# Optimization experiments

Measured on AMD Instinct MI355X. Metric: run time of the kernel, lower is better.

## Reference

```python
import jax, jax.numpy as jnp
import numpy as np

NBLOCK = 2000
DIM = 2048
B, T = 32, 1024
EPS = 1e-12  # F.normalize eps


def _l2norm(v, axis):
    n = jnp.sqrt(jnp.sum(v * v, axis=axis, keepdims=True))
    return v / jnp.maximum(n, EPS)


def setup_inputs() -> dict:
    key = jax.random.key(0)
    kx, km, kw = jax.random.split(key, 3)
    x = jax.random.normal(kx, (B, T, DIM), dtype=jnp.float32)
    mask = jax.random.randint(km, (B, T), 0, 2).astype(jnp.int32)
    stdv = 1.0 / np.sqrt(DIM)
    weight = jax.random.uniform(kw, (NBLOCK, DIM), dtype=jnp.float32,
                                minval=-stdv, maxval=stdv)
    return {"x": x, "mask": mask, "weight": weight}


def reference(x, mask, weight):
    half = x.shape[0] // 2
    nblock = weight.shape[0]
    m = mask.astype(x.dtype)  # [B, T]

    # diversity: || W W^T - I ||_F
    gram = weight @ weight.T  # [N, N]
    diversity_loss = jnp.linalg.norm(gram - jnp.eye(nblock, dtype=weight.dtype))

    # cosine-similarity attention: [B, T, N]
    att = jnp.einsum('btd,nd->btn', _l2norm(x, axis=2), _l2norm(weight, axis=1))

    # uniformity loss: masked sum over T, softmax over blocks, mean over half-batch
    s = jnp.einsum('btn,bt->nb', att[:half], m[:half])  # [N, half]
    tmp = jnp.mean(jax.nn.softmax(s, axis=0), axis=1)   # [N]
    u_loss = jnp.linalg.norm(tmp)

    # per-row min over masked positions of the top-1 similarity
    top1 = jnp.max(att, axis=2)  # [B, T] (only topk[...,0] is used)
    inf = jnp.asarray(jnp.inf, dtype=x.dtype)
    masked_top1 = jnp.where(m > 0, top1, inf)
    min_sim = jnp.min(masked_top1[:half], axis=1)   # [half]
    ab_min = jnp.min(masked_top1[half:], axis=1)    # [half]

    return (0.2 * diversity_loss,
            2.0 - jnp.mean(min_sim) + jnp.mean(ab_min),
            0.5 * u_loss)
```

## Files before the change

kernel.cpp:

```cpp
#include <hip/hip_runtime.h>

typedef unsigned short u16;
typedef unsigned int u32;
typedef __attribute__((ext_vector_type(8))) short short8;
typedef __attribute__((ext_vector_type(8))) u16 ushort8;
typedef __attribute__((ext_vector_type(4))) float fx4;

#define DIMK 2048
#define NBLK 2000

typedef const __attribute__((address_space(1))) void* gp_t;
typedef __attribute__((address_space(3))) void* lp_t;

__device__ __forceinline__ u16 f2bf(float f) {
  u32 u = __float_as_uint(f);
  u32 r = (u + 0x7fffu + ((u >> 16) & 1u)) >> 16;
  return (u16)r;
}

__device__ __forceinline__ u32 fkey(float f) {
  u32 u = __float_as_uint(f);
  return (u & 0x80000000u) ? ~u : (u | 0x80000000u);
}
__device__ __forceinline__ float dekey(u32 k) {
  u32 u = (k & 0x80000000u) ? (k ^ 0x80000000u) : ~k;
  return __uint_as_float(u);
}

__device__ __forceinline__ void gemm_tile(const u16* __restrict__ Abase,
                                          const u16* __restrict__ Bbase,
                                          int row0, int col0,
                                          u16* lsA, u16* lsB,
                                          fx4 acc[4][4])
{
  const int tid  = threadIdx.x;
  const int wv   = tid >> 6;
  const int lane = tid & 63;
  const int wr   = wv & 1, wc = wv >> 1;
  const int quad = lane >> 4, lc = lane & 15;

  const int srow = wv * 32 + (lane >> 2);
  const int skel = (lane & 3) * 8;
  const u16* gA0 = Abase + (size_t)(row0 + srow) * DIMK + skel;
  const u16* gA1 = Abase + (size_t)(row0 + srow + 16) * DIMK + skel;
  const u16* gB0 = Bbase + (size_t)(col0 + srow) * DIMK + skel;
  const u16* gB1 = Bbase + (size_t)(col0 + srow + 16) * DIMK + skel;
  u16* lA0 = lsA + wv * 1024;
  u16* lA1 = lsA + wv * 1024 + 512;
  u16* lB0 = lsB + wv * 1024;
  u16* lB1 = lsB + wv * 1024 + 512;

  const int fA = (wr * 64 + lc) * 32 + quad * 8;
  const int fB = (wc * 64 + lc) * 32 + quad * 8;

#pragma unroll
  for (int mi = 0; mi < 4; mi++)
#pragma unroll
    for (int ni = 0; ni < 4; ni++)
      acc[mi][ni] = fx4{0.f, 0.f, 0.f, 0.f};

  for (int k0 = 0; k0 < DIMK; k0 += 32) {
    __syncthreads();
    __builtin_amdgcn_global_load_lds((gp_t)gA0, (lp_t)lA0, 16, 0, 0);
    __builtin_amdgcn_global_load_lds((gp_t)gA1, (lp_t)lA1, 16, 0, 0);
    __builtin_amdgcn_global_load_lds((gp_t)gB0, (lp_t)lB0, 16, 0, 0);
    __builtin_amdgcn_global_load_lds((gp_t)gB1, (lp_t)lB1, 16, 0, 0);
    gA0 += 32; gA1 += 32; gB0 += 32; gB1 += 32;
    __syncthreads();
    short8 af[4], bfr[4];
#pragma unroll
    for (int mi = 0; mi < 4; mi++)
      af[mi] = *(const short8*)(lsA + fA + mi * 512);
#pragma unroll
    for (int ni = 0; ni < 4; ni++)
      bfr[ni] = *(const short8*)(lsB + fB + ni * 512);
#pragma unroll
    for (int mi = 0; mi < 4; mi++)
#pragma unroll
      for (int ni = 0; ni < 4; ni++)
        acc[mi][ni] = __builtin_amdgcn_mfma_f32_16x16x32_bf16(af[mi], bfr[ni], acc[mi][ni], 0, 0, 0);
  }
}

__global__ __launch_bounds__(256) void norm_rows_x(const float* __restrict__ x,
                                                   u16* __restrict__ Xn)
{
  const int row = blockIdx.x;
  const int tid = threadIdx.x;
  __shared__ float red[4];
  const float4* xr = (const float4*)(x + (size_t)row * DIMK);
  float4 v0 = xr[2 * tid];
  float4 v1 = xr[2 * tid + 1];
  float ss = v0.x*v0.x + v0.y*v0.y + v0.z*v0.z + v0.w*v0.w
           + v1.x*v1.x + v1.y*v1.y + v1.z*v1.z + v1.w*v1.w;
#pragma unroll
  for (int off = 1; off < 64; off <<= 1) ss += __shfl_xor(ss, off);
  if ((tid & 63) == 0) red[tid >> 6] = ss;
  __syncthreads();
  ss = red[0] + red[1] + red[2] + red[3];
  float inv = 1.0f / fmaxf(sqrtf(ss), 1e-12f);
  ushort8 o;
  o[0] = f2bf(v0.x * inv); o[1] = f2bf(v0.y * inv);
  o[2] = f2bf(v0.z * inv); o[3] = f2bf(v0.w * inv);
  o[4] = f2bf(v1.x * inv); o[5] = f2bf(v1.y * inv);
  o[6] = f2bf(v1.z * inv); o[7] = f2bf(v1.w * inv);
  ((ushort8*)(Xn + (size_t)row * DIMK))[tid] = o;
}

__global__ __launch_bounds__(256) void norm_rows_w(const float* __restrict__ w,
                                                   u16* __restrict__ Wn,
                                                   u16* __restrict__ Wb)
{
  const int row = blockIdx.x;
  const int tid = threadIdx.x;
  __shared__ float red[4];
  if (row < NBLK) {
    const float4* wr_ = (const float4*)(w + (size_t)row * DIMK);
    float4 v0 = wr_[2 * tid];
    float4 v1 = wr_[2 * tid + 1];
    float ss = v0.x*v0.x + v0.y*v0.y + v0.z*v0.z + v0.w*v0.w
             + v1.x*v1.x + v1.y*v1.y + v1.z*v1.z + v1.w*v1.w;
#pragma unroll
    for (int off = 1; off < 64; off <<= 1) ss += __shfl_xor(ss, off);
    if ((tid & 63) == 0) red[tid >> 6] = ss;
    __syncthreads();
    ss = red[0] + red[1] + red[2] + red[3];
    float inv = 1.0f / fmaxf(sqrtf(ss), 1e-12f);
    ushort8 on, ob;
    on[0] = f2bf(v0.x * inv); on[1] = f2bf(v0.y * inv);
    on[2] = f2bf(v0.z * inv); on[3] = f2bf(v0.w * inv);
    on[4] = f2bf(v1.x * inv); on[5] = f2bf(v1.y * inv);
    on[6] = f2bf(v1.z * inv); on[7] = f2bf(v1.w * inv);
    ob[0] = f2bf(v0.x); ob[1] = f2bf(v0.y); ob[2] = f2bf(v0.z); ob[3] = f2bf(v0.w);
    ob[4] = f2bf(v1.x); ob[5] = f2bf(v1.y); ob[6] = f2bf(v1.z); ob[7] = f2bf(v1.w);
    ((ushort8*)(Wn + (size_t)row * DIMK))[tid] = on;
    ((ushort8*)(Wb + (size_t)row * DIMK))[tid] = ob;
  } else {
    ushort8 z = ushort8{0, 0, 0, 0, 0, 0, 0, 0};
    ((ushort8*)(Wn + (size_t)row * DIMK))[tid] = z;
    ((ushort8*)(Wb + (size_t)row * DIMK))[tid] = z;
  }
}

__global__ __launch_bounds__(256) void gram_kernel(const u16* __restrict__ Wb,
                                                   float* __restrict__ divsum)
{
  __shared__ __align__(16) u16 lsA[4096];
  __shared__ __align__(16) u16 lsB[4096];
  fx4 acc[4][4];
  const int i0 = blockIdx.y * 128, j0 = blockIdx.x * 128;
  gemm_tile(Wb, Wb, i0, j0, lsA, lsB, acc);
  const int tid = threadIdx.x, wv = tid >> 6, lane = tid & 63;
  const int wr = wv & 1, wc = wv >> 1, quad = lane >> 4, lc = lane & 15;
  float local = 0.f;
#pragma unroll
  for (int mi = 0; mi < 4; mi++) {
#pragma unroll
    for (int ni = 0; ni < 4; ni++) {
#pragma unroll
      for (int r = 0; r < 4; r++) {
        int i = i0 + wr * 64 + mi * 16 + quad * 4 + r;
        int j = j0 + wc * 64 + ni * 16 + lc;
        float g = acc[mi][ni][r];
        float d = (i == j && i < NBLK) ? 1.0f : 0.0f;
        float e = g - d;
        local += e * e;
      }
    }
  }
#pragma unroll
  for (int off = 1; off < 64; off <<= 1) local += __shfl_xor(local, off);
  if (lane == 0) atomicAdd(divsum, local);
}

__global__ __launch_bounds__(256) void att_kernel(const u16* __restrict__ Xn,
                                                  const u16* __restrict__ Wn,
                                                  const int* __restrict__ mask,
                                                  u32* __restrict__ top1k,
                                                  float* __restrict__ s)
{
  __shared__ __align__(16) u16 lsA[4096];
  __shared__ __align__(16) u16 lsB[4096];
  __shared__ float sMask[128];
  const int xb = blockIdx.x, yb = blockIdx.y;
  const int tid = threadIdx.x;
  if (tid < 128) sMask[tid] = (float)mask[yb * 128 + tid];
  fx4 acc[4][4];
  gemm_tile(Xn, Wn, yb * 128, xb * 128, lsA, lsB, acc);
  const int wv = tid >> 6, lane = tid & 63;
  const int wr = wv & 1, wc = wv >> 1, quad = lane >> 4, lc = lane & 15;
  const int colbase = xb * 128 + wc * 64;

#pragma unroll
  for (int mi = 0; mi < 4; mi++) {
#pragma unroll
    for (int r = 0; r < 4; r++) {
      float v = -3.0e38f;
#pragma unroll
      for (int ni = 0; ni < 4; ni++) {
        int col = colbase + ni * 16 + lc;
        float av = acc[mi][ni][r];
        v = (col < NBLK && av > v) ? av : v;
      }
      v = fmaxf(v, __shfl_xor(v, 1));
      v = fmaxf(v, __shfl_xor(v, 2));
      v = fmaxf(v, __shfl_xor(v, 4));
      v = fmaxf(v, __shfl_xor(v, 8));
      if (lc == 0) {
        int row = yb * 128 + wr * 64 + mi * 16 + quad * 4 + r;
        atomicMax(&top1k[row], fkey(v));
      }
    }
  }

  if (yb < 128) {
    const int b = yb >> 3;
#pragma unroll
    for (int ni = 0; ni < 4; ni++) {
      float sv = 0.f;
#pragma unroll
      for (int mi = 0; mi < 4; mi++) {
#pragma unroll
        for (int r = 0; r < 4; r++)
          sv += sMask[wr * 64 + mi * 16 + quad * 4 + r] * acc[mi][ni][r];
      }
      sv += __shfl_xor(sv, 16);
      sv += __shfl_xor(sv, 32);
      int col = colbase + ni * 16 + lc;
      if (quad == 0 && col < NBLK)
        atomicAdd(&s[b * 2048 + col], sv);
    }
  }
}

__global__ __launch_bounds__(256) void softmax_kernel(const float* __restrict__ s,
                                                      float* __restrict__ tmp)
{
  const int b = blockIdx.x, tid = threadIdx.x;
  const float* sb = s + b * 2048;
  __shared__ float red[4];
  float mx = -3.0e38f;
  for (int n = tid; n < NBLK; n += 256) mx = fmaxf(mx, sb[n]);
#pragma unroll
  for (int off = 1; off < 64; off <<= 1) mx = fmaxf(mx, __shfl_xor(mx, off));
  if ((tid & 63) == 0) red[tid >> 6] = mx;
  __syncthreads();
  mx = fmaxf(fmaxf(red[0], red[1]), fmaxf(red[2], red[3]));
  __syncthreads();
  float se = 0.f;
  for (int n = tid; n < NBLK; n += 256) se += expf(sb[n] - mx);
#pragma unroll
  for (int off = 1; off < 64; off <<= 1) se += __shfl_xor(se, off);
  if ((tid & 63) == 0) red[tid >> 6] = se;
  __syncthreads();
  se = red[0] + red[1] + red[2] + red[3];
  float scale = 1.0f / (se * 16.0f);
  for (int n = tid; n < NBLK; n += 256) atomicAdd(&tmp[n], expf(sb[n] - mx) * scale);
}

__global__ __launch_bounds__(1024) void finalize_kernel(const u32* __restrict__ top1k,
                                                        const int* __restrict__ mask,
                                                        const float* __restrict__ tmp,
                                                        const float* __restrict__ divsum,
                                                        float* __restrict__ out)
{
  const int tid = threadIdx.x;
  __shared__ float sMin[32];
  __shared__ float sSq[16];
  const int b = tid >> 5, li = tid & 31;
  float mn = 3.0e38f;
  for (int t = li; t < 1024; t += 32) {
    int idx = b * 1024 + t;
    if (mask[idx] > 0) mn = fminf(mn, dekey(top1k[idx]));
  }
#pragma unroll
  for (int off = 1; off < 32; off <<= 1) mn = fminf(mn, __shfl_xor(mn, off));
  if (li == 0) sMin[b] = mn;
  float ssq = 0.f;
  for (int n = tid; n < NBLK; n += 1024) { float v = tmp[n]; ssq += v * v; }
#pragma unroll
  for (int off = 1; off < 64; off <<= 1) ssq += __shfl_xor(ssq, off);
  if ((tid & 63) == 0) sSq[tid >> 6] = ssq;
  __syncthreads();
  if (tid == 0) {
    float m0 = 0.f, m1 = 0.f;
    for (int i = 0; i < 16; i++) { m0 += sMin[i]; m1 += sMin[16 + i]; }
    m0 *= (1.0f / 16.0f); m1 *= (1.0f / 16.0f);
    float sq = 0.f;
    for (int i = 0; i < 16; i++) sq += sSq[i];
    out[0] = 0.2f * sqrtf(divsum[0]);
    out[1] = 2.0f - m0 + m1;
    out[2] = 0.5f * sqrtf(sq);
  }
}

extern "C" void kernel_launch(void* const* d_in, const int* in_sizes, int n_in,
                              void* d_out, int out_size, void* d_ws, size_t ws_size,
                              hipStream_t stream) {
  const float* x    = (const float*)d_in[0];
  const int*   mask = (const int*)d_in[1];
  const float* w    = (const float*)d_in[2];
  float* out = (float*)d_out;

  char* ws = (char*)d_ws;
  u32*   top1k  = (u32*)(ws);
  float* s      = (float*)(ws + 131072);
  float* tmp    = (float*)(ws + 262144);
  float* divsum = (float*)(ws + 270336);
  u16*   Xn     = (u16*)(ws + 270592);
  u16*   Wn     = (u16*)(ws + 270592 + 134217728ull);
  u16*   Wb     = (u16*)(ws + 270592 + 134217728ull + 8388608ull);

  hipMemsetAsync(ws, 0, 270592, stream);

  norm_rows_w<<<dim3(2048), dim3(256), 0, stream>>>(w, Wn, Wb);
  norm_rows_x<<<dim3(32768), dim3(256), 0, stream>>>(x, Xn);
  gram_kernel<<<dim3(16, 16), dim3(256), 0, stream>>>(Wb, divsum);
  att_kernel<<<dim3(16, 256), dim3(256), 0, stream>>>(Xn, Wn, mask, top1k, s);
  softmax_kernel<<<dim3(16), dim3(256), 0, stream>>>(s, tmp);
  finalize_kernel<<<dim3(1), dim3(1024), 0, stream>>>(top1k, mask, tmp, divsum, out);
}
```

Before: 794.1 us.

## Re-layout GEMM LDS staging for conflict-free fragment reads; one-wave-per-row normalization

The global-to-LDS staging pattern in the shared GEMM tile now maps lanes to rows first and k-chunks second. Fragment reads then hit contiguous 16-lane groups, which is meant to cut LDS bank conflicts in both the gram and attention GEMMs. The row-normalization kernels now assign one wavefront per row with 8 float4 loads per lane. This drops the LDS reduction and __syncthreads and cuts block count fourfold, at the cost of narrower 8-byte stores.

```diff
diff --git a/kernel.cpp b/kernel.cpp
--- a/kernel.cpp
+++ b/kernel.cpp
@@ -4,6 +4,7 @@
 typedef unsigned int u32;
 typedef __attribute__((ext_vector_type(8))) short short8;
 typedef __attribute__((ext_vector_type(8))) u16 ushort8;
+typedef __attribute__((ext_vector_type(4))) u16 ushort4_t;
 typedef __attribute__((ext_vector_type(4))) float fx4;
 
 #define DIMK 2048
@@ -39,19 +40,18 @@
   const int wr   = wv & 1, wc = wv >> 1;
   const int quad = lane >> 4, lc = lane & 15;
 
-  const int srow = wv * 32 + (lane >> 2);
-  const int skel = (lane & 3) * 8;
+  const int srow = wv * 32 + (lane & 15);
+  const int skel = (lane >> 4) * 8;
   const u16* gA0 = Abase + (size_t)(row0 + srow) * DIMK + skel;
-  const u16* gA1 = Abase + (size_t)(row0 + srow + 16) * DIMK + skel;
+  const u16* gA1 = gA0 + (size_t)16 * DIMK;
   const u16* gB0 = Bbase + (size_t)(col0 + srow) * DIMK + skel;
-  const u16* gB1 = Bbase + (size_t)(col0 + srow + 16) * DIMK + skel;
+  const u16* gB1 = gB0 + (size_t)16 * DIMK;
   u16* lA0 = lsA + wv * 1024;
   u16* lA1 = lsA + wv * 1024 + 512;
   u16* lB0 = lsB + wv * 1024;
   u16* lB1 = lsB + wv * 1024 + 512;
 
-  const int fA = (wr * 64 + lc) * 32 + quad * 8;
-  const int fB = (wc * 64 + lc) * 32 + quad * 8;
+  const int fIntra = quad * 128 + lc * 8;
 
 #pragma unroll
   for (int mi = 0; mi < 4; mi++)
@@ -70,10 +70,10 @@
     short8 af[4], bfr[4];
 #pragma unroll
     for (int mi = 0; mi < 4; mi++)
-      af[mi] = *(const short8*)(lsA + fA + mi * 512);
+      af[mi] = *(const short8*)(lsA + (wr * 4 + mi) * 512 + fIntra);
 #pragma unroll
     for (int ni = 0; ni < 4; ni++)
-      bfr[ni] = *(const short8*)(lsB + fB + ni * 512);
+      bfr[ni] = *(const short8*)(lsB + (wc * 4 + ni) * 512 + fIntra);
 #pragma unroll
     for (int mi = 0; mi < 4; mi++)
 #pragma unroll
@@ -85,60 +85,63 @@
 __global__ __launch_bounds__(256) void norm_rows_x(const float* __restrict__ x,
                                                    u16* __restrict__ Xn)
 {
-  const int row = blockIdx.x;
-  const int tid = threadIdx.x;
-  __shared__ float red[4];
+  const int wv = threadIdx.x >> 6, lane = threadIdx.x & 63;
+  const int row = blockIdx.x * 4 + wv;
   const float4* xr = (const float4*)(x + (size_t)row * DIMK);
-  float4 v0 = xr[2 * tid];
-  float4 v1 = xr[2 * tid + 1];
-  float ss = v0.x*v0.x + v0.y*v0.y + v0.z*v0.z + v0.w*v0.w
-           + v1.x*v1.x + v1.y*v1.y + v1.z*v1.z + v1.w*v1.w;
+  float4 v[8];
+  float ss = 0.f;
+#pragma unroll
+  for (int j = 0; j < 8; j++) {
+    v[j] = xr[j * 64 + lane];
+    ss += v[j].x*v[j].x + v[j].y*v[j].y + v[j].z*v[j].z + v[j].w*v[j].w;
+  }
 #pragma unroll
   for (int off = 1; off < 64; off <<= 1) ss += __shfl_xor(ss, off);
-  if ((tid & 63) == 0) red[tid >> 6] = ss;
-  __syncthreads();
-  ss = red[0] + red[1] + red[2] + red[3];
   float inv = 1.0f / fmaxf(sqrtf(ss), 1e-12f);
-  ushort8 o;
-  o[0] = f2bf(v0.x * inv); o[1] = f2bf(v0.y * inv);
-  o[2] = f2bf(v0.z * inv); o[3] = f2bf(v0.w * inv);
-  o[4] = f2bf(v1.x * inv); o[5] = f2bf(v1.y * inv);
-  o[6] = f2bf(v1.z * inv); o[7] = f2bf(v1.w * inv);
-  ((ushort8*)(Xn + (size_t)row * DIMK))[tid] = o;
+  ushort4_t* o = (ushort4_t*)(Xn + (size_t)row * DIMK);
+#pragma unroll
+  for (int j = 0; j < 8; j++) {
+    ushort4_t t;
+    t[0] = f2bf(v[j].x * inv); t[1] = f2bf(v[j].y * inv);
+    t[2] = f2bf(v[j].z * inv); t[3] = f2bf(v[j].w * inv);
+    o[j * 64 + lane] = t;
+  }
 }
 
 __global__ __launch_bounds__(256) void norm_rows_w(const float* __restrict__ w,
                                                    u16* __restrict__ Wn,
                                                    u16* __restrict__ Wb)
 {
-  const int row = blockIdx.x;
-  const int tid = threadIdx.x;
-  __shared__ float red[4];
+  const int wv = threadIdx.x >> 6, lane = threadIdx.x & 63;
+  const int row = blockIdx.x * 4 + wv;
+  ushort4_t* on_ = (ushort4_t*)(Wn + (size_t)row * DIMK);
+  ushort4_t* ob_ = (ushort4_t*)(Wb + (size_t)row * DIMK);
   if (row < NBLK) {
     const float4* wr_ = (const float4*)(w + (size_t)row * DIMK);
-    float4 v0 = wr_[2 * tid];
-    float4 v1 = wr_[2 * tid + 1];
-    float ss = v0.x*v0.x + v0.y*v0.y + v0.z*v0.z + v0.w*v0.w
-             + v1.x*v1.x + v1.y*v1.y + v1.z*v1.z + v1.w*v1.w;
+    float4 v[8];
+    float ss = 0.f;
+#pragma unroll
+    for (int j = 0; j < 8; j++) {
+      v[j] = wr_[j * 64 + lane];
+      ss += v[j].x*v[j].x + v[j].y*v[j].y + v[j].z*v[j].z + v[j].w*v[j].w;
+    }
 #pragma unroll
     for (int off = 1; off < 64; off <<= 1) ss += __shfl_xor(ss, off);
-    if ((tid & 63) == 0) red[tid >> 6] = ss;
-    __syncthreads();
-    ss = red[0] + red[1] + red[2] + red[3];
     float inv = 1.0f / fmaxf(sqrtf(ss), 1e-12f);
-    ushort8 on, ob;
-    on[0] = f2bf(v0.x * inv); on[1] = f2bf(v0.y * inv);
-    on[2] = f2bf(v0.z * inv); on[3] = f2bf(v0.w * inv);
-    on[4] = f2bf(v1.x * inv); on[5] = f2bf(v1.y * inv);
-    on[6] = f2bf(v1.z * inv); on[7] = f2bf(v1.w * inv);
-    ob[0] = f2bf(v0.x); ob[1] = f2bf(v0.y); ob[2] = f2bf(v0.z); ob[3] = f2bf(v0.w);
-    ob[4] = f2bf(v1.x); ob[5] = f2bf(v1.y); ob[6] = f2bf(v1.z); ob[7] = f2bf(v1.w);
-    ((ushort8*)(Wn + (size_t)row * DIMK))[tid] = on;
-    ((ushort8*)(Wb + (size_t)row * DIMK))[tid] = ob;
+#pragma unroll
+    for (int j = 0; j < 8; j++) {
+      ushort4_t tn, tb;
+      tn[0] = f2bf(v[j].x * inv); tn[1] = f2bf(v[j].y * inv);
+      tn[2] = f2bf(v[j].z * inv); tn[3] = f2bf(v[j].w * inv);
+      tb[0] = f2bf(v[j].x); tb[1] = f2bf(v[j].y);
+      tb[2] = f2bf(v[j].z); tb[3] = f2bf(v[j].w);
+      on_[j * 64 + lane] = tn;
+      ob_[j * 64 + lane] = tb;
+    }
   } else {
-    ushort8 z = ushort8{0, 0, 0, 0, 0, 0, 0, 0};
-    ((ushort8*)(Wn + (size_t)row * DIMK))[tid] = z;
-    ((ushort8*)(Wb + (size_t)row * DIMK))[tid] = z;
+    ushort4_t z = ushort4_t{0, 0, 0, 0};
+#pragma unroll
+    for (int j = 0; j < 8; j++) { on_[j * 64 + lane] = z; ob_[j * 64 + lane] = z; }
   }
 }
 
@@ -313,8 +316,8 @@
 
   hipMemsetAsync(ws, 0, 270592, stream);
 
-  norm_rows_w<<<dim3(2048), dim3(256), 0, stream>>>(w, Wn, Wb);
-  norm_rows_x<<<dim3(32768), dim3(256), 0, stream>>>(x, Xn);
+  norm_rows_w<<<dim3(512), dim3(256), 0, stream>>>(w, Wn, Wb);
+  norm_rows_x<<<dim3(8192), dim3(256), 0, stream>>>(x, Xn);
   gram_kernel<<<dim3(16, 16), dim3(256), 0, stream>>>(Wb, divsum);
   att_kernel<<<dim3(16, 256), dim3(256), 0, stream>>>(Xn, Wn, mask, top1k, s);
   softmax_kernel<<<dim3(16), dim3(256), 0, stream>>>(s, tmp);
```

Result: slower. 989.3 us (+24.6%).
